# Performance work log

Hardware: AMD Instinct MI355X
Metric: run time of the kernel (lower is better)

Reference implementation:

```python
import jax, jax.numpy as jnp
import numpy as np

_B = 128          # quantization block size
FP8_MAX = 448.0   # finfo(float8_e4m3fn).max


def _quantize_weight_block(w):
    """w: [N, K] fp32 -> (fp8 weight [N,K], per-block scale [N/128, K/128])."""
    N, K = w.shape
    blk = w.reshape(N // _B, _B, K // _B, _B).transpose(0, 2, 1, 3)  # [n,k,128,128]
    amax = jnp.abs(blk).max(axis=(-2, -1))
    scale = jnp.maximum(amax / FP8_MAX, 1e-12).astype(jnp.float32)   # [n,k]
    q = jnp.clip(blk / scale[:, :, None, None], -FP8_MAX, FP8_MAX).astype(jnp.float8_e4m3fn)
    wq = q.transpose(0, 2, 1, 3).reshape(N, K)
    return wq, scale


def _dequant_weight(wq, scale):
    N, K = wq.shape
    blk = wq.reshape(N // _B, _B, K // _B, _B).astype(jnp.float32)
    blk = blk * scale[:, None, :, None]
    return blk.reshape(N, K)


def _fake_quant_act(x):
    """Per-token, per-128-column-group fp8 fake quantization. x: [M, K]."""
    M, K = x.shape
    xg = x.reshape(M, K // _B, _B)
    amax = jnp.abs(xg).max(axis=-1, keepdims=True)
    scale = jnp.maximum(amax / FP8_MAX, 1e-12)
    xq = jnp.clip(xg / scale, -FP8_MAX, FP8_MAX).astype(jnp.float8_e4m3fn).astype(jnp.float32)
    return (xq * scale).reshape(M, K)


def _fq_linear(x, wq, wscale):
    # fake-quant activation, dequant weight, high-precision GEMM
    return _fake_quant_act(x) @ _dequant_weight(wq, wscale).T


def setup_inputs() -> dict:
    key = jax.random.key(0)
    k0, k1, k2, k3 = jax.random.split(key, 4)
    M, H, I = 4096, 4096, 14336
    x = jax.random.normal(k0, (M, H), dtype=jnp.float32)
    gate_w = jax.random.normal(k1, (I, H), dtype=jnp.float32) * 0.05
    up_w = jax.random.normal(k2, (I, H), dtype=jnp.float32) * 0.05
    down_w = jax.random.normal(k3, (H, I), dtype=jnp.float32) * 0.05
    gq, gs = _quantize_weight_block(gate_w)
    uq, us = _quantize_weight_block(up_w)
    dq, ds = _quantize_weight_block(down_w)
    return {
        "x": x,
        "gate_weight": gq, "gate_weight_scale": gs,
        "up_weight": uq, "up_weight_scale": us,
        "down_weight": dq, "down_weight_scale": ds,
    }


def reference(x, gate_weight, gate_weight_scale, up_weight, up_weight_scale,
              down_weight, down_weight_scale):
    gate_out = _fq_linear(x, gate_weight, gate_weight_scale)
    up_out = _fq_linear(x, up_weight, up_weight_scale)
    hidden = jax.nn.silu(gate_out) * up_out
    return _fq_linear(hidden, down_weight, down_weight_scale)
```

## Files before the change

kernel.cpp:

```cpp
#include <hip/hip_runtime.h>

typedef float floatx4 __attribute__((ext_vector_type(4)));
typedef long longx2 __attribute__((ext_vector_type(2)));
typedef unsigned int u32;
typedef unsigned char u8;

#define MDIM 4096
#define HDIM 4096
#define IDIM 14336
#define FP8MAX 448.0f

__device__ __forceinline__ int swz4(int r) { return (r ^ (r >> 2)) & 3; }
__device__ __forceinline__ int frag_off(int row, int quad) {
  return (row << 6) + ((quad ^ swz4(row)) << 4);
}

__device__ __forceinline__ void gload16(const u8* g, u8* l) {
  __builtin_amdgcn_global_load_lds((const __attribute__((address_space(1))) u32*)g,
                                   (__attribute__((address_space(3))) u32*)l, 16, 0, 0);
}

#define VMW(n) asm volatile("s_waitcnt vmcnt(" #n ")" ::: "memory")
#define BAR() __builtin_amdgcn_s_barrier()

__global__ void detect_dtype(const unsigned int* __restrict__ w, int* __restrict__ flag) {
  if (threadIdx.x == 0 && blockIdx.x == 0) {
    bool f32 = true, b16 = true;
    for (int i = 0; i < 64; ++i) {
      const unsigned int v = w[i];
      if (v & 0xFFFFFu) f32 = false;
      if ((v & 0xFu) || ((v >> 16) & 0xFu)) b16 = false;
    }
    *flag = f32 ? 2 : (b16 ? 1 : 0);
  }
}

__device__ __forceinline__ float bfu(unsigned int bits16) {
  union { unsigned int u; float f; } c;
  c.u = bits16 << 16;
  return c.f;
}

__device__ __forceinline__ unsigned int pack2(unsigned int lo, unsigned int hi) {
  int pk = __builtin_amdgcn_cvt_pk_fp8_f32(bfu(lo & 0xFFFFu), bfu(lo >> 16), 0, false);
  pk = __builtin_amdgcn_cvt_pk_fp8_f32(bfu(hi & 0xFFFFu), bfu(hi >> 16), pk, true);
  return (unsigned int)pk;
}

__global__ __launch_bounds__(256) void conv_w(const void* __restrict__ src,
                                              unsigned char* __restrict__ dst,
                                              const int* __restrict__ flag_p) {
  const int flag = *flag_p;
  if (flag == 0) return;
  const long t = (long)blockIdx.x * 256 + threadIdx.x;
  uint4 out;
  if (flag == 2) {
    const float4* s = (const float4*)src;
    unsigned int o[4];
#pragma unroll
    for (int p = 0; p < 4; ++p) {
      const float4 v = s[t * 4 + p];
      int pk = __builtin_amdgcn_cvt_pk_fp8_f32(v.x, v.y, 0, false);
      pk = __builtin_amdgcn_cvt_pk_fp8_f32(v.z, v.w, pk, true);
      o[p] = (unsigned int)pk;
    }
    out = make_uint4(o[0], o[1], o[2], o[3]);
  } else {
    const uint4* s = (const uint4*)src;
    const uint4 a = s[t * 2], b = s[t * 2 + 1];
    out = make_uint4(pack2(a.x, a.y), pack2(a.z, a.w),
                     pack2(b.x, b.y), pack2(b.z, b.w));
  }
  ((uint4*)dst)[t] = out;
}

__global__ __launch_bounds__(256) void fq_act(const float* __restrict__ x,
                                              unsigned char* __restrict__ xq,
                                              float* __restrict__ xsT) {
  const int tid = threadIdx.x;
  const int lane = tid & 63, w = tid >> 6;
  const int g = blockIdx.x * 4 + w;
  const int row = g >> 5, kb = g & 31;

  const float2 v = ((const float2*)(x + (size_t)row * HDIM + kb * 128))[lane];
  float amax = fmaxf(fabsf(v.x), fabsf(v.y));
#pragma unroll
  for (int off = 1; off < 64; off <<= 1)
    amax = fmaxf(amax, __shfl_xor(amax, off, 64));

  const float scale = fmaxf(amax / FP8MAX, 1e-12f);
  const float q0 = fminf(fmaxf(v.x / scale, -FP8MAX), FP8MAX);
  const float q1 = fminf(fmaxf(v.y / scale, -FP8MAX), FP8MAX);
  const int pk = __builtin_amdgcn_cvt_pk_fp8_f32(q0, q1, 0, false);
  ((unsigned short*)(xq + (size_t)row * HDIM + kb * 128))[lane] = (unsigned short)(pk & 0xFFFF);
  if (lane == 0) xsT[(size_t)kb * MDIM + row] = scale;
}

__global__ __launch_bounds__(256, 2)
void dual_gemm_silu_fq(const u8* __restrict__ xq, const float* __restrict__ xsT,
                       const u8* __restrict__ gw_cv, const u8* __restrict__ gw_raw,
                       const float* __restrict__ gs,
                       const u8* __restrict__ uw_cv, const u8* __restrict__ uw_raw,
                       const float* __restrict__ us,
                       u8* __restrict__ hq, float* __restrict__ hsT,
                       const int* __restrict__ flag_p, const int use_conv) {
  __shared__ __align__(16) u8 lds[73728];

  const int tid = threadIdx.x;
  const int lane = tid & 63, wid = tid >> 6;
  const int quad = lane >> 4, l16 = lane & 15;

  const int bid0 = blockIdx.x;
  const int bid = (bid0 & 7) * 448 + (bid0 >> 3);
  const int mi = bid & 31, ni = bid >> 5;
  const size_t m0 = (size_t)mi << 7, n0 = (size_t)ni << 7;

  const u8* gw = gw_raw;
  const u8* uw = uw_raw;
  if (use_conv) {
    if (*flag_p != 0) { gw = gw_cv; uw = uw_cv; }
  }

  const u8* baseA = xq + m0 * HDIM;
  const u8* baseG = gw + n0 * HDIM;
  const u8* baseU = uw + n0 * HDIM;

  const int r16 = lane >> 2, slot = lane & 3;
  u32 srcoff[2], dstoff[2];
#pragma unroll
  for (int i = 0; i < 2; ++i) {
    const int row = wid * 32 + i * 16 + r16;
    srcoff[i] = (u32)(row * HDIM) + (u32)((slot ^ swz4(row)) << 4);
    dstoff[i] = (u32)(wid * 2048 + i * 1024);
  }

  int offA[2], offB[8];
#pragma unroll
  for (int mt = 0; mt < 2; ++mt) offA[mt] = frag_off(wid * 32 + mt * 16 + l16, quad);
#pragma unroll
  for (int nt = 0; nt < 8; ++nt) offB[nt] = frag_off(nt * 16 + l16, quad);

  floatx4 accG[2][8], accU[2][8];
#pragma unroll
  for (int mt = 0; mt < 2; ++mt)
#pragma unroll
    for (int nt = 0; nt < 8; ++nt) {
      accG[mt][nt] = {0.f, 0.f, 0.f, 0.f};
      accU[mt][nt] = {0.f, 0.f, 0.f, 0.f};
    }

  auto STAGE = [&](int t, int b) {
    const u32 ko = (u32)t << 6;
    u8* lb = lds + b * 24576;
#pragma unroll
    for (int i = 0; i < 2; ++i) {
      gload16(baseA + srcoff[i] + ko, lb + dstoff[i]);
      gload16(baseG + srcoff[i] + ko, lb + 8192u + dstoff[i]);
      gload16(baseU + srcoff[i] + ko, lb + 16384u + dstoff[i]);
    }
  };

  auto HALF = [&](int b) {
    const u8* lb = lds + b * 24576;
    const u8* bufA = lb;
    const u8* bufG = lb + 8192;
    const u8* bufU = lb + 16384;
    longx2 aF[2];
#pragma unroll
    for (int mt = 0; mt < 2; ++mt) aF[mt] = *(const longx2*)(bufA + offA[mt]);

    __builtin_amdgcn_s_setprio(1);
#pragma unroll
    for (int nt = 0; nt < 8; ++nt) {
      const longx2 bF = *(const longx2*)(bufG + offB[nt]);
#pragma unroll
      for (int mt = 0; mt < 2; ++mt) {
        accG[mt][nt] = __builtin_amdgcn_mfma_f32_16x16x32_fp8_fp8(aF[mt][0], bF[0], accG[mt][nt], 0, 0, 0);
        accG[mt][nt] = __builtin_amdgcn_mfma_f32_16x16x32_fp8_fp8(aF[mt][1], bF[1], accG[mt][nt], 0, 0, 0);
      }
    }
#pragma unroll
    for (int nt = 0; nt < 8; ++nt) {
      const longx2 bF = *(const longx2*)(bufU + offB[nt]);
#pragma unroll
      for (int mt = 0; mt < 2; ++mt) {
        accU[mt][nt] = __builtin_amdgcn_mfma_f32_16x16x32_fp8_fp8(aF[mt][0], bF[0], accU[mt][nt], 0, 0, 0);
        accU[mt][nt] = __builtin_amdgcn_mfma_f32_16x16x32_fp8_fp8(aF[mt][1], bF[1], accU[mt][nt], 0, 0, 0);
      }
    }
    __builtin_amdgcn_s_setprio(0);
  };

  const float* xsBase = xsT + m0 + wid * 32 + quad * 4;
  floatx4 xv0 = *(const floatx4*)(xsBase);
  floatx4 xv1 = *(const floatx4*)(xsBase + 16);
  float sgn = gs[ni * 32];
  float sun = us[ni * 32];

  STAGE(0, 0);
  STAGE(1, 1);

  floatx4 prX[2];
  float sgp = 1.f, sup = 1.f;
  int cb = 0;

  for (int kb = 0; kb < 32; ++kb) {
    {
      int sb = cb + 2; if (sb >= 3) sb -= 3;
      if (kb < 31) STAGE(2 * kb + 2, sb);
      const floatx4 cx0 = xv0, cx1 = xv1;
      const float sgc = sgn, suc = sun;
      if (kb) {
        const float rgs = sgp * __builtin_amdgcn_rcpf(sgc);
        const float rus = sup * __builtin_amdgcn_rcpf(suc);
        floatx4 i0, i1;
#pragma unroll
        for (int r = 0; r < 4; ++r) {
          i0[r] = __builtin_amdgcn_rcpf(cx0[r]);
          i1[r] = __builtin_amdgcn_rcpf(cx1[r]);
        }
        const floatx4 cm0 = prX[0] * i0, cm1 = prX[1] * i1;
        const floatx4 rg0 = cm0 * rgs, ru0 = cm0 * rus;
        const floatx4 rg1 = cm1 * rgs, ru1 = cm1 * rus;
#pragma unroll
        for (int nt = 0; nt < 8; ++nt) {
          accG[0][nt] *= rg0;
          accG[1][nt] *= rg1;
          accU[0][nt] *= ru0;
          accU[1][nt] *= ru1;
        }
      }
      prX[0] = cx0; prX[1] = cx1;
      sgp = sgc; sup = suc;
      const int kbn = kb < 31 ? kb + 1 : 31;
      const float* xn = xsBase + (size_t)kbn * MDIM;
      xv0 = *(const floatx4*)(xn);
      xv1 = *(const floatx4*)(xn + 16);
      sgn = gs[ni * 32 + kbn];
      sun = us[ni * 32 + kbn];

      if (kb < 31) { VMW(12); } else { VMW(6); }
      BAR();
      HALF(cb);
      BAR();
      if (++cb >= 3) cb = 0;
    }
    {
      int sb = cb + 2; if (sb >= 3) sb -= 3;
      if (kb < 31) {
        STAGE(2 * kb + 3, sb);
        VMW(12);
      } else {
        VMW(0);
      }
      BAR();
      HALF(cb);
      BAR();
      if (++cb >= 3) cb = 0;
    }
  }

#pragma unroll
  for (int mt = 0; mt < 2; ++mt) {
    const floatx4 fg = prX[mt] * sgp;
    const floatx4 fu = prX[mt] * sup;
#pragma unroll
    for (int nt = 0; nt < 8; ++nt) {
      accG[mt][nt] *= fg;
      accU[mt][nt] *= fu;
    }
  }

  u8* ot = lds;
#pragma unroll
  for (int mt = 0; mt < 2; ++mt) {
    float h[8][4];
    float amax[4] = {0.f, 0.f, 0.f, 0.f};
#pragma unroll
    for (int nt = 0; nt < 8; ++nt)
#pragma unroll
      for (int r = 0; r < 4; ++r) {
        const float gv = accG[mt][nt][r];
        const float uv = accU[mt][nt][r];
        const float hv = (gv / (1.f + __expf(-gv))) * uv;
        h[nt][r] = hv;
        amax[r] = fmaxf(amax[r], fabsf(hv));
      }
#pragma unroll
    for (int off = 1; off < 16; off <<= 1)
#pragma unroll
      for (int r = 0; r < 4; ++r)
        amax[r] = fmaxf(amax[r], __shfl_xor(amax[r], off, 64));

    float scale[4];
#pragma unroll
    for (int r = 0; r < 4; ++r) scale[r] = fmaxf(amax[r] / FP8MAX, 1e-12f);

    const int rowl = wid * 32 + mt * 16 + quad * 4;
    if (l16 == 0) {
#pragma unroll
      for (int r = 0; r < 4; ++r)
        hsT[(size_t)ni * MDIM + m0 + rowl + r] = scale[r];
    }
#pragma unroll
    for (int nt = 0; nt < 8; ++nt)
#pragma unroll
      for (int r = 0; r < 4; ++r) {
        const float q = fminf(fmaxf(h[nt][r] / scale[r], -FP8MAX), FP8MAX);
        const int pk = __builtin_amdgcn_cvt_pk_fp8_f32(q, 0.f, 0, false);
        ot[(rowl + r) * 128 + nt * 16 + l16] = (u8)(pk & 0xFF);
      }
  }
  __syncthreads();
  {
    const int row = tid >> 1, half = tid & 1;
    const uint4* s = (const uint4*)(ot + row * 128 + half * 64);
    uint4* d = (uint4*)(hq + (m0 + row) * IDIM + n0 + half * 64);
#pragma unroll
    for (int i = 0; i < 4; ++i) d[i] = s[i];
  }
}

__global__ __launch_bounds__(256, 2)
void gemm_down(const u8* __restrict__ hq, const float* __restrict__ hsT,
               const u8* __restrict__ dw_cv, const u8* __restrict__ dw_raw,
               const float* __restrict__ dsc, float* __restrict__ out,
               const int* __restrict__ flag_p, const int use_conv) {
  __shared__ __align__(16) u8 lds[49152];

  const int tid = threadIdx.x;
  const int lane = tid & 63, wid = tid >> 6;
  const int quad = lane >> 4, l16 = lane & 15;

  const int bid0 = blockIdx.x;
  const int bid = (bid0 & 7) * 128 + (bid0 >> 3);
  const int mi = bid & 31, ni = bid >> 5;
  const size_t m0 = (size_t)mi << 7, n0 = (size_t)ni << 7;

  const u8* dw = dw_raw;
  if (use_conv) {
    if (*flag_p != 0) dw = dw_cv;
  }

  const u8* baseA = hq + m0 * IDIM;
  const u8* baseB = dw + n0 * IDIM;

  const int r16 = lane >> 2, slot = lane & 3;
  u32 srcoff[2], dstoff[2];
#pragma unroll
  for (int i = 0; i < 2; ++i) {
    const int row = wid * 32 + i * 16 + r16;
    srcoff[i] = (u32)(row * IDIM) + (u32)((slot ^ swz4(row)) << 4);
    dstoff[i] = (u32)(wid * 2048 + i * 1024);
  }

  int offA[2], offB[8];
#pragma unroll
  for (int mt = 0; mt < 2; ++mt) offA[mt] = frag_off(wid * 32 + mt * 16 + l16, quad);
#pragma unroll
  for (int nt = 0; nt < 8; ++nt) offB[nt] = frag_off(nt * 16 + l16, quad);

  floatx4 acc[2][8];
#pragma unroll
  for (int mt = 0; mt < 2; ++mt)
#pragma unroll
    for (int nt = 0; nt < 8; ++nt) acc[mt][nt] = {0.f, 0.f, 0.f, 0.f};

  auto STAGE = [&](int t, int b) {
    const u32 ko = (u32)t << 6;
    u8* lb = lds + b * 16384;
#pragma unroll
    for (int i = 0; i < 2; ++i) {
      gload16(baseA + srcoff[i] + ko, lb + dstoff[i]);
      gload16(baseB + srcoff[i] + ko, lb + 8192u + dstoff[i]);
    }
  };

  auto HALF = [&](int b) {
    const u8* lb = lds + b * 16384;
    longx2 aF[2];
#pragma unroll
    for (int mt = 0; mt < 2; ++mt) aF[mt] = *(const longx2*)(lb + offA[mt]);
    __builtin_amdgcn_s_setprio(1);
#pragma unroll
    for (int nt = 0; nt < 8; ++nt) {
      const longx2 bF = *(const longx2*)(lb + 8192 + offB[nt]);
#pragma unroll
      for (int mt = 0; mt < 2; ++mt) {
        acc[mt][nt] = __builtin_amdgcn_mfma_f32_16x16x32_fp8_fp8(aF[mt][0], bF[0], acc[mt][nt], 0, 0, 0);
        acc[mt][nt] = __builtin_amdgcn_mfma_f32_16x16x32_fp8_fp8(aF[mt][1], bF[1], acc[mt][nt], 0, 0, 0);
      }
    }
    __builtin_amdgcn_s_setprio(0);
  };

  const float* hsBase = hsT + m0 + wid * 32 + quad * 4;
  floatx4 xv0 = *(const floatx4*)(hsBase);
  floatx4 xv1 = *(const floatx4*)(hsBase + 16);
  float sdn = dsc[ni * 112];

  STAGE(0, 0);
  STAGE(1, 1);

  floatx4 prX[2];
  float sdp = 1.f;
  int cb = 0;

  for (int kb = 0; kb < 112; ++kb) {
    {
      int sb = cb + 2; if (sb >= 3) sb -= 3;
      if (kb < 111) STAGE(2 * kb + 2, sb);
      const floatx4 cx0 = xv0, cx1 = xv1;
      const float sdc = sdn;
      if (kb) {
        const float rds = sdp * __builtin_amdgcn_rcpf(sdc);
        floatx4 i0, i1;
#pragma unroll
        for (int r = 0; r < 4; ++r) {
          i0[r] = __builtin_amdgcn_rcpf(cx0[r]);
          i1[r] = __builtin_amdgcn_rcpf(cx1[r]);
        }
        const floatx4 r0 = prX[0] * i0 * rds;
        const floatx4 r1 = prX[1] * i1 * rds;
#pragma unroll
        for (int nt = 0; nt < 8; ++nt) {
          acc[0][nt] *= r0;
          acc[1][nt] *= r1;
        }
      }
      prX[0] = cx0; prX[1] = cx1;
      sdp = sdc;
      const int kbn = kb < 111 ? kb + 1 : 111;
      const float* xn = hsBase + (size_t)kbn * MDIM;
      xv0 = *(const floatx4*)(xn);
      xv1 = *(const floatx4*)(xn + 16);
      sdn = dsc[ni * 112 + kbn];

      if (kb < 111) { VMW(8); } else { VMW(4); }
      BAR();
      HALF(cb);
      BAR();
      if (++cb >= 3) cb = 0;
    }
    {
      int sb = cb + 2; if (sb >= 3) sb -= 3;
      if (kb < 111) {
        STAGE(2 * kb + 3, sb);
        VMW(8);
      } else {
        VMW(0);
      }
      BAR();
      HALF(cb);
      BAR();
      if (++cb >= 3) cb = 0;
    }
  }

#pragma unroll
  for (int mt = 0; mt < 2; ++mt) {
    const int rowl = wid * 32 + mt * 16 + quad * 4;
#pragma unroll
    for (int nt = 0; nt < 8; ++nt)
#pragma unroll
      for (int r = 0; r < 4; ++r)
        out[(m0 + rowl + r) * (size_t)HDIM + n0 + nt * 16 + l16] =
            acc[mt][nt][r] * prX[mt][r] * sdp;
  }
}

extern "C" void kernel_launch(void* const* d_in, const int* in_sizes, int n_in,
                              void* d_out, int out_size, void* d_ws, size_t ws_size,
                              hipStream_t stream) {
  const float* x   = (const float*)d_in[0];
  const void* gw_s = d_in[1];
  const float* gs  = (const float*)d_in[2];
  const void* uw_s = d_in[3];
  const float* us  = (const float*)d_in[4];
  const void* dw_s = d_in[5];
  const float* dsc = (const float*)d_in[6];
  float* out       = (float*)d_out;

  const size_t NW = (size_t)IDIM * HDIM;

  unsigned char* ws = (unsigned char*)d_ws;
  unsigned char* xq = ws;
  float* xsT = (float*)(ws + 16777216);
  unsigned char* hq  = ws + 17301504;
  float* hsT = (float*)(ws + 76021760);
  unsigned char* gwq = ws + 77856768;
  unsigned char* uwq = ws + 136577024;
  unsigned char* dwq = gwq;
  int* flag = (int*)(ws + 195297280);

  const bool fits = ws_size >= (size_t)195297284;
  const int use_conv = fits ? 1 : 0;

  const int convBlocks = (int)(NW / (16 * 256));

  if (fits) {
    detect_dtype<<<1, 64, 0, stream>>>((const unsigned int*)gw_s, flag);
    conv_w<<<convBlocks, 256, 0, stream>>>(gw_s, gwq, flag);
    conv_w<<<convBlocks, 256, 0, stream>>>(uw_s, uwq, flag);
  }
  fq_act<<<(MDIM * (HDIM / 128)) / 4, 256, 0, stream>>>(x, xq, xsT);
  dual_gemm_silu_fq<<<(MDIM / 128) * (IDIM / 128), 256, 0, stream>>>(
      xq, xsT, gwq, (const unsigned char*)gw_s, gs,
      uwq, (const unsigned char*)uw_s, us, hq, hsT, flag, use_conv);
  if (fits) {
    conv_w<<<convBlocks, 256, 0, stream>>>(dw_s, dwq, flag);
  }
  gemm_down<<<(MDIM / 128) * (HDIM / 128), 256, 0, stream>>>(
      hq, hsT, dwq, (const unsigned char*)dw_s, dsc, out, flag, use_conv);
}
```

Before: 1.765 ms.

## Enlarge GEMM block tiles to 256 rows with 512-thread blocks

Both GEMMs now use 512-thread blocks. The gate/up kernel moves to a 256x128 tile and the down kernel to a 256x256 tile, with each wave in the down kernel holding a 32x256 accumulator. Staging is rewritten so each thread issues one 16-byte load per operand row-slot, and the down kernel tracks two weight-scale columns per tile. The goal is to halve how often weights (and, in the down GEMM, activations) are reloaded across blocks, raising arithmetic intensity. In exchange, LDS per block grows to 96 KB. The launch bounds of (512, 2) also cap register use per thread, so the doubled accumulator arrays risk spilling.

Result: slower. 1.848 ms (+4.7%).

```diff
diff --git a/kernel.cpp b/kernel.cpp
--- a/kernel.cpp
+++ b/kernel.cpp
@@ -96,7 +96,7 @@
   if (lane == 0) xsT[(size_t)kb * MDIM + row] = scale;
 }
 
-__global__ __launch_bounds__(256, 2)
+__global__ __launch_bounds__(512, 2)
 void dual_gemm_silu_fq(const u8* __restrict__ xq, const float* __restrict__ xsT,
                        const u8* __restrict__ gw_cv, const u8* __restrict__ gw_raw,
                        const float* __restrict__ gs,
@@ -104,16 +104,16 @@
                        const float* __restrict__ us,
                        u8* __restrict__ hq, float* __restrict__ hsT,
                        const int* __restrict__ flag_p, const int use_conv) {
-  __shared__ __align__(16) u8 lds[73728];
+  __shared__ __align__(16) u8 lds[98304];
 
   const int tid = threadIdx.x;
   const int lane = tid & 63, wid = tid >> 6;
   const int quad = lane >> 4, l16 = lane & 15;
 
   const int bid0 = blockIdx.x;
-  const int bid = (bid0 & 7) * 448 + (bid0 >> 3);
-  const int mi = bid & 31, ni = bid >> 5;
-  const size_t m0 = (size_t)mi << 7, n0 = (size_t)ni << 7;
+  const int bid = (bid0 & 7) * 224 + (bid0 >> 3);
+  const int mi = bid & 15, ni = bid >> 4;
+  const size_t m0 = (size_t)mi << 8, n0 = (size_t)ni << 7;
 
   const u8* gw = gw_raw;
   const u8* uw = uw_raw;
@@ -125,14 +125,16 @@
   const u8* baseG = gw + n0 * HDIM;
   const u8* baseU = uw + n0 * HDIM;
 
-  const int r16 = lane >> 2, slot = lane & 3;
-  u32 srcoff[2], dstoff[2];
-#pragma unroll
-  for (int i = 0; i < 2; ++i) {
-    const int row = wid * 32 + i * 16 + r16;
-    srcoff[i] = (u32)(row * HDIM) + (u32)((slot ^ swz4(row)) << 4);
-    dstoff[i] = (u32)(wid * 2048 + i * 1024);
-  }
+  const int srow = tid >> 2, slot = tid & 3;
+  u32 srcA[2], dstA[2];
+#pragma unroll
+  for (int p = 0; p < 2; ++p) {
+    const int row = p * 128 + srow;
+    srcA[p] = (u32)(row * HDIM) + (u32)((slot ^ swz4(row)) << 4);
+    dstA[p] = (u32)(p * 8192 + tid * 16);
+  }
+  const u32 srcW = (u32)(srow * HDIM) + (u32)((slot ^ swz4(srow)) << 4);
+  const u32 dstW = (u32)(tid * 16);
 
   int offA[2], offB[8];
 #pragma unroll
@@ -151,20 +153,18 @@
 
   auto STAGE = [&](int t, int b) {
     const u32 ko = (u32)t << 6;
-    u8* lb = lds + b * 24576;
-#pragma unroll
-    for (int i = 0; i < 2; ++i) {
-      gload16(baseA + srcoff[i] + ko, lb + dstoff[i]);
-      gload16(baseG + srcoff[i] + ko, lb + 8192u + dstoff[i]);
-      gload16(baseU + srcoff[i] + ko, lb + 16384u + dstoff[i]);
-    }
+    u8* lb = lds + b * 32768;
+    gload16(baseA + srcA[0] + ko, lb + dstA[0]);
+    gload16(baseA + srcA[1] + ko, lb + dstA[1]);
+    gload16(baseG + srcW + ko, lb + 16384u + dstW);
+    gload16(baseU + srcW + ko, lb + 24576u + dstW);
   };
 
   auto HALF = [&](int b) {
-    const u8* lb = lds + b * 24576;
+    const u8* lb = lds + b * 32768;
     const u8* bufA = lb;
-    const u8* bufG = lb + 8192;
-    const u8* bufU = lb + 16384;
+    const u8* bufG = lb + 16384;
+    const u8* bufU = lb + 24576;
     longx2 aF[2];
 #pragma unroll
     for (int mt = 0; mt < 2; ++mt) aF[mt] = *(const longx2*)(bufA + offA[mt]);
@@ -239,7 +239,7 @@
       sgn = gs[ni * 32 + kbn];
       sun = us[ni * 32 + kbn];
 
-      if (kb < 31) { VMW(12); } else { VMW(6); }
+      if (kb < 31) { VMW(12); } else { VMW(8); }
       BAR();
       HALF(cb);
       BAR();
@@ -321,21 +321,21 @@
   }
 }
 
-__global__ __launch_bounds__(256, 2)
+__global__ __launch_bounds__(512, 2)
 void gemm_down(const u8* __restrict__ hq, const float* __restrict__ hsT,
                const u8* __restrict__ dw_cv, const u8* __restrict__ dw_raw,
                const float* __restrict__ dsc, float* __restrict__ out,
                const int* __restrict__ flag_p, const int use_conv) {
-  __shared__ __align__(16) u8 lds[49152];
+  __shared__ __align__(16) u8 lds[98304];
 
   const int tid = threadIdx.x;
   const int lane = tid & 63, wid = tid >> 6;
   const int quad = lane >> 4, l16 = lane & 15;
 
   const int bid0 = blockIdx.x;
-  const int bid = (bid0 & 7) * 128 + (bid0 >> 3);
-  const int mi = bid & 31, ni = bid >> 5;
-  const size_t m0 = (size_t)mi << 7, n0 = (size_t)ni << 7;
+  const int bid = (bid0 & 7) * 32 + (bid0 >> 3);
+  const int mi = bid & 15, ni = bid >> 4;
+  const size_t m0 = (size_t)mi << 8, n0 = (size_t)ni << 8;
 
   const u8* dw = dw_raw;
   if (use_conv) {
@@ -345,46 +345,46 @@
   const u8* baseA = hq + m0 * IDIM;
   const u8* baseB = dw + n0 * IDIM;
 
-  const int r16 = lane >> 2, slot = lane & 3;
-  u32 srcoff[2], dstoff[2];
-#pragma unroll
-  for (int i = 0; i < 2; ++i) {
-    const int row = wid * 32 + i * 16 + r16;
-    srcoff[i] = (u32)(row * IDIM) + (u32)((slot ^ swz4(row)) << 4);
-    dstoff[i] = (u32)(wid * 2048 + i * 1024);
-  }
-
-  int offA[2], offB[8];
+  const int srow = tid >> 2, slot = tid & 3;
+  u32 srcR[2], dstR[2];
+#pragma unroll
+  for (int p = 0; p < 2; ++p) {
+    const int row = p * 128 + srow;
+    srcR[p] = (u32)(row * IDIM) + (u32)((slot ^ swz4(row)) << 4);
+    dstR[p] = (u32)(p * 8192 + tid * 16);
+  }
+
+  int offA[2], offB[16];
 #pragma unroll
   for (int mt = 0; mt < 2; ++mt) offA[mt] = frag_off(wid * 32 + mt * 16 + l16, quad);
 #pragma unroll
-  for (int nt = 0; nt < 8; ++nt) offB[nt] = frag_off(nt * 16 + l16, quad);
-
-  floatx4 acc[2][8];
+  for (int nt = 0; nt < 16; ++nt) offB[nt] = frag_off(nt * 16 + l16, quad);
+
+  floatx4 acc[2][16];
 #pragma unroll
   for (int mt = 0; mt < 2; ++mt)
 #pragma unroll
-    for (int nt = 0; nt < 8; ++nt) acc[mt][nt] = {0.f, 0.f, 0.f, 0.f};
+    for (int nt = 0; nt < 16; ++nt) acc[mt][nt] = {0.f, 0.f, 0.f, 0.f};
 
   auto STAGE = [&](int t, int b) {
     const u32 ko = (u32)t << 6;
-    u8* lb = lds + b * 16384;
-#pragma unroll
-    for (int i = 0; i < 2; ++i) {
-      gload16(baseA + srcoff[i] + ko, lb + dstoff[i]);
-      gload16(baseB + srcoff[i] + ko, lb + 8192u + dstoff[i]);
-    }
+    u8* lb = lds + b * 32768;
+    gload16(baseA + srcR[0] + ko, lb + dstR[0]);
+    gload16(baseA + srcR[1] + ko, lb + dstR[1]);
+    gload16(baseB + srcR[0] + ko, lb + 16384u + dstR[0]);
+    gload16(baseB + srcR[1] + ko, lb + 16384u + dstR[1]);
   };
 
   auto HALF = [&](int b) {
-    const u8* lb = lds + b * 16384;
+    const u8* lb = lds + b * 32768;
+    const u8* bufB = lb + 16384;
     longx2 aF[2];
 #pragma unroll
     for (int mt = 0; mt < 2; ++mt) aF[mt] = *(const longx2*)(lb + offA[mt]);
     __builtin_amdgcn_s_setprio(1);
 #pragma unroll
-    for (int nt = 0; nt < 8; ++nt) {
-      const longx2 bF = *(const longx2*)(lb + 8192 + offB[nt]);
+    for (int nt = 0; nt < 16; ++nt) {
+      const longx2 bF = *(const longx2*)(bufB + offB[nt]);
 #pragma unroll
       for (int mt = 0; mt < 2; ++mt) {
         acc[mt][nt] = __builtin_amdgcn_mfma_f32_16x16x32_fp8_fp8(aF[mt][0], bF[0], acc[mt][nt], 0, 0, 0);
@@ -397,13 +397,14 @@
   const float* hsBase = hsT + m0 + wid * 32 + quad * 4;
   floatx4 xv0 = *(const floatx4*)(hsBase);
   floatx4 xv1 = *(const floatx4*)(hsBase + 16);
-  float sdn = dsc[ni * 112];
+  float sdn0 = dsc[(2 * ni) * 112];
+  float sdn1 = dsc[(2 * ni + 1) * 112];
 
   STAGE(0, 0);
   STAGE(1, 1);
 
   floatx4 prX[2];
-  float sdp = 1.f;
+  float sd0p = 1.f, sd1p = 1.f;
   int cb = 0;
 
   for (int kb = 0; kb < 112; ++kb) {
@@ -411,32 +412,37 @@
       int sb = cb + 2; if (sb >= 3) sb -= 3;
       if (kb < 111) STAGE(2 * kb + 2, sb);
       const floatx4 cx0 = xv0, cx1 = xv1;
-      const float sdc = sdn;
+      const float sd0c = sdn0, sd1c = sdn1;
       if (kb) {
-        const float rds = sdp * __builtin_amdgcn_rcpf(sdc);
+        const float rd0 = sd0p * __builtin_amdgcn_rcpf(sd0c);
+        const float rd1 = sd1p * __builtin_amdgcn_rcpf(sd1c);
         floatx4 i0, i1;
 #pragma unroll
         for (int r = 0; r < 4; ++r) {
           i0[r] = __builtin_amdgcn_rcpf(cx0[r]);
           i1[r] = __builtin_amdgcn_rcpf(cx1[r]);
         }
-        const floatx4 r0 = prX[0] * i0 * rds;
-        const floatx4 r1 = prX[1] * i1 * rds;
-#pragma unroll
-        for (int nt = 0; nt < 8; ++nt) {
-          acc[0][nt] *= r0;
-          acc[1][nt] *= r1;
+        const floatx4 cm0 = prX[0] * i0, cm1 = prX[1] * i1;
+        const floatx4 r00 = cm0 * rd0, r01 = cm0 * rd1;
+        const floatx4 r10 = cm1 * rd0, r11 = cm1 * rd1;
+#pragma unroll
+      for (int nt = 0; nt < 8; ++nt) {
+          acc[0][nt] *= r00;
+          acc[1][nt] *= r10;
+          acc[0][nt + 8] *= r01;
+          acc[1][nt + 8] *= r11;
         }
       }
       prX[0] = cx0; prX[1] = cx1;
-      sdp = sdc;
+      sd0p = sd0c; sd1p = sd1c;
       const int kbn = kb < 111 ? kb + 1 : 111;
       const float* xn = hsBase + (size_t)kbn * MDIM;
       xv0 = *(const floatx4*)(xn);
       xv1 = *(const floatx4*)(xn + 16);
-      sdn = dsc[ni * 112 + kbn];
-
-      if (kb < 111) { VMW(8); } else { VMW(4); }
+      sdn0 = dsc[(2 * ni) * 112 + kbn];
+      sdn1 = dsc[(2 * ni + 1) * 112 + kbn];
+
+      if (kb < 111) { VMW(12); } else { VMW(8); }
       BAR();
       HALF(cb);
       BAR();
@@ -446,7 +452,7 @@
       int sb = cb + 2; if (sb >= 3) sb -= 3;
       if (kb < 111) {
         STAGE(2 * kb + 3, sb);
-        VMW(8);
+        VMW(12);
       } else {
         VMW(0);
       }
@@ -461,11 +467,13 @@
   for (int mt = 0; mt < 2; ++mt) {
     const int rowl = wid * 32 + mt * 16 + quad * 4;
 #pragma unroll
-    for (int nt = 0; nt < 8; ++nt)
+    for (int nt = 0; nt < 16; ++nt) {
+      const float sdf = (nt < 8) ? sd0p : sd1p;
 #pragma unroll
       for (int r = 0; r < 4; ++r)
         out[(m0 + rowl + r) * (size_t)HDIM + n0 + nt * 16 + l16] =
-            acc[mt][nt][r] * prX[mt][r] * sdp;
+            acc[mt][nt][r] * prX[mt][r] * sdf;
+    }
   }
 }
 
@@ -504,12 +512,12 @@
     conv_w<<<convBlocks, 256, 0, stream>>>(uw_s, uwq, flag);
   }
   fq_act<<<(MDIM * (HDIM / 128)) / 4, 256, 0, stream>>>(x, xq, xsT);
-  dual_gemm_silu_fq<<<(MDIM / 128) * (IDIM / 128), 256, 0, stream>>>(
+  dual_gemm_silu_fq<<<(MDIM / 256) * (IDIM / 128), 512, 0, stream>>>(
       xq, xsT, gwq, (const unsigned char*)gw_s, gs,
       uwq, (const unsigned char*)uw_s, us, hq, hsT, flag, use_conv);
   if (fits) {
     conv_w<<<convBlocks, 256, 0, stream>>>(dw_s, dwq, flag);
   }
-  gemm_down<<<(MDIM / 128) * (HDIM / 128), 256, 0, stream>>>(
+  gemm_down<<<(MDIM / 256) * (HDIM / 256), 512, 0, stream>>>(
       hq, hsT, dwq, (const unsigned char*)dw_s, dsc, out, flag, use_conv);
 }
```

## Widen down-projection GEMM tile to 128x256 with two weight-scale groups

Applied to the files above, without the earlier changes.

The down-projection GEMM tile grows from 128x128 to 128x256 output, so each block loads twice as many weight rows per K step and each A fragment is reused across 16 N subtiles. The grid halves to 512 blocks, LDS per block rises to 72KB across three stages, accumulators double to 32 floatx4, and per-128-column weight scales are tracked as two groups. The aim is to raise arithmetic intensity and cut redundant activation loads. The costs are higher register pressure that may break two-blocks-per-CU occupancy, fewer blocks for load balancing, and retuned vmcnt waits.

Result: no change. 1.755 ms (-0.6%).

```diff
diff --git a/kernel.cpp b/kernel.cpp
--- a/kernel.cpp
+++ b/kernel.cpp
@@ -326,16 +326,16 @@
                const u8* __restrict__ dw_cv, const u8* __restrict__ dw_raw,
                const float* __restrict__ dsc, float* __restrict__ out,
                const int* __restrict__ flag_p, const int use_conv) {
-  __shared__ __align__(16) u8 lds[49152];
+  __shared__ __align__(16) u8 lds[73728];
 
   const int tid = threadIdx.x;
   const int lane = tid & 63, wid = tid >> 6;
   const int quad = lane >> 4, l16 = lane & 15;
 
   const int bid0 = blockIdx.x;
-  const int bid = (bid0 & 7) * 128 + (bid0 >> 3);
+  const int bid = (bid0 & 7) * 64 + (bid0 >> 3);
   const int mi = bid & 31, ni = bid >> 5;
-  const size_t m0 = (size_t)mi << 7, n0 = (size_t)ni << 7;
+  const size_t m0 = (size_t)mi << 7, n0 = (size_t)ni << 8;
 
   const u8* dw = dw_raw;
   if (use_conv) {
@@ -346,45 +346,51 @@
   const u8* baseB = dw + n0 * IDIM;
 
   const int r16 = lane >> 2, slot = lane & 3;
-  u32 srcoff[2], dstoff[2];
-#pragma unroll
-  for (int i = 0; i < 2; ++i) {
-    const int row = wid * 32 + i * 16 + r16;
-    srcoff[i] = (u32)(row * IDIM) + (u32)((slot ^ swz4(row)) << 4);
-    dstoff[i] = (u32)(wid * 2048 + i * 1024);
-  }
-
-  int offA[2], offB[8];
+  u32 srcA[2], srcB[4];
+#pragma unroll
+  for (int p = 0; p < 2; ++p) {
+    const int row = p * 64 + wid * 16 + r16;
+    srcA[p] = (u32)(row * IDIM) + (u32)((slot ^ swz4(row)) << 4);
+  }
+#pragma unroll
+  for (int p = 0; p < 4; ++p) {
+    const int row = p * 64 + wid * 16 + r16;
+    srcB[p] = (u32)(row * IDIM) + (u32)((slot ^ swz4(row)) << 4);
+  }
+
+  int offA[2], offB[16];
 #pragma unroll
   for (int mt = 0; mt < 2; ++mt) offA[mt] = frag_off(wid * 32 + mt * 16 + l16, quad);
 #pragma unroll
-  for (int nt = 0; nt < 8; ++nt) offB[nt] = frag_off(nt * 16 + l16, quad);
-
-  floatx4 acc[2][8];
+  for (int nt = 0; nt < 16; ++nt) offB[nt] = frag_off(nt * 16 + l16, quad);
+
+  floatx4 acc[2][16];
 #pragma unroll
   for (int mt = 0; mt < 2; ++mt)
 #pragma unroll
-    for (int nt = 0; nt < 8; ++nt) acc[mt][nt] = {0.f, 0.f, 0.f, 0.f};
+    for (int nt = 0; nt < 16; ++nt) acc[mt][nt] = {0.f, 0.f, 0.f, 0.f};
 
   auto STAGE = [&](int t, int b) {
     const u32 ko = (u32)t << 6;
-    u8* lb = lds + b * 16384;
-#pragma unroll
-    for (int i = 0; i < 2; ++i) {
-      gload16(baseA + srcoff[i] + ko, lb + dstoff[i]);
-      gload16(baseB + srcoff[i] + ko, lb + 8192u + dstoff[i]);
-    }
+    u8* lb = lds + b * 24576;
+#pragma unroll
+    for (int p = 0; p < 2; ++p)
+      gload16(baseA + srcA[p] + ko, lb + (u32)(p * 4096 + wid * 1024));
+#pragma unroll
+    for (int p = 0; p < 4; ++p)
+      gload16(baseB + srcB[p] + ko, lb + 8192u + (u32)(p * 4096 + wid * 1024));
   };
 
   auto HALF = [&](int b) {
-    const u8* lb = lds + b * 16384;
+    const u8* lb = lds + b * 24576;
+    const u8* bufB = lb + 8192;
     longx2 aF[2];
 #pragma unroll
     for (int mt = 0; mt < 2; ++mt) aF[mt] = *(const longx2*)(lb + offA[mt]);
     __builtin_amdgcn_s_setprio(1);
 #pragma unroll
-    for (int nt = 0; nt < 8; ++nt) {
-      const longx2 bF = *(const longx2*)(lb + 8192 + offB[nt]);
+    for (int nt = 0; nt < 16; ++nt) {
+      const longx2 bF = *(const longx2*)(bufB + offB[nt]);
 #pragma unroll
       for (int mt = 0; mt < 2; ++mt) {
         acc[mt][nt] = __builtin_amdgcn_mfma_f32_16x16x32_fp8_fp8(aF[mt][0], bF[0], acc[mt][nt], 0, 0, 0);
@@ -397,13 +403,14 @@
   const float* hsBase = hsT + m0 + wid * 32 + quad * 4;
   floatx4 xv0 = *(const floatx4*)(hsBase);
   floatx4 xv1 = *(const floatx4*)(hsBase + 16);
-  float sdn = dsc[ni * 112];
+  float sdn0 = dsc[(2 * ni) * 112];
+  float sdn1 = dsc[(2 * ni + 1) * 112];
 
   STAGE(0, 0);
   STAGE(1, 1);
 
   floatx4 prX[2];
-  float sdp = 1.f;
+  float sd0p = 1.f, sd1p = 1.f;
   int cb = 0;
 
   for (int kb = 0; kb < 112; ++kb) {
@@ -411,32 +418,37 @@
       int sb = cb + 2; if (sb >= 3) sb -= 3;
       if (kb < 111) STAGE(2 * kb + 2, sb);
       const floatx4 cx0 = xv0, cx1 = xv1;
-      const float sdc = sdn;
+      const float sd0c = sdn0, sd1c = sdn1;
       if (kb) {
-        const float rds = sdp * __builtin_amdgcn_rcpf(sdc);
+        const float rd0 = sd0p * __builtin_amdgcn_rcpf(sd0c);
+        const float rd1 = sd1p * __builtin_amdgcn_rcpf(sd1c);
         floatx4 i0, i1;
 #pragma unroll
         for (int r = 0; r < 4; ++r) {
           i0[r] = __builtin_amdgcn_rcpf(cx0[r]);
           i1[r] = __builtin_amdgcn_rcpf(cx1[r]);
         }
-        const floatx4 r0 = prX[0] * i0 * rds;
-        const floatx4 r1 = prX[1] * i1 * rds;
+        const floatx4 cm0 = prX[0] * i0, cm1 = prX[1] * i1;
+        const floatx4 r00 = cm0 * rd0, r01 = cm0 * rd1;
+        const floatx4 r10 = cm1 * rd0, r11 = cm1 * rd1;
 #pragma unroll
         for (int nt = 0; nt < 8; ++nt) {
-          acc[0][nt] *= r0;
-          acc[1][nt] *= r1;
+          acc[0][nt] *= r00;
+          acc[1][nt] *= r10;
+          acc[0][nt + 8] *= r01;
+          acc[1][nt + 8] *= r11;
         }
       }
       prX[0] = cx0; prX[1] = cx1;
-      sdp = sdc;
+      sd0p = sd0c; sd1p = sd1c;
       const int kbn = kb < 111 ? kb + 1 : 111;
       const float* xn = hsBase + (size_t)kbn * MDIM;
       xv0 = *(const floatx4*)(xn);
       xv1 = *(const floatx4*)(xn + 16);
-      sdn = dsc[ni * 112 + kbn];
-
-      if (kb < 111) { VMW(8); } else { VMW(4); }
+      sdn0 = dsc[(2 * ni) * 112 + kbn];
+      sdn1 = dsc[(2 * ni + 1) * 112 + kbn];
+
+      if (kb == 0) { VMW(8); } else if (kb < 111) { VMW(12); } else { VMW(8); }
       BAR();
       HALF(cb);
       BAR();
@@ -446,7 +458,7 @@
       int sb = cb + 2; if (sb >= 3) sb -= 3;
       if (kb < 111) {
         STAGE(2 * kb + 3, sb);
-        VMW(8);
+        VMW(12);
       } else {
         VMW(0);
       }
@@ -461,11 +473,13 @@
   for (int mt = 0; mt < 2; ++mt) {
     const int rowl = wid * 32 + mt * 16 + quad * 4;
 #pragma unroll
-    for (int nt = 0; nt < 8; ++nt)
+    for (int nt = 0; nt < 16; ++nt) {
+      const float sdf = (nt < 8) ? sd0p : sd1p;
 #pragma unroll
       for (int r = 0; r < 4; ++r)
         out[(m0 + rowl + r) * (size_t)HDIM + n0 + nt * 16 + l16] =
-            acc[mt][nt][r] * prX[mt][r] * sdp;
+            acc[mt][nt][r] * prX[mt][r] * sdf;
+    }
   }
 }
 
@@ -510,6 +524,6 @@
   if (fits) {
     conv_w<<<convBlocks, 256, 0, stream>>>(dw_s, dwq, flag);
   }
-  gemm_down<<<(MDIM / 128) * (HDIM / 128), 256, 0, stream>>>(
+  gemm_down<<<(MDIM / 128) * (HDIM / 256), 256, 0, stream>>>(
       hq, hsT, dwq, (const unsigned char*)dw_s, dsc, out, flag, use_conv);
 }
```
